# Kernel tuning notes

Hardware: AMD Instinct MI355X
Metric: run time of the kernel (lower is better)

## Reference

```python
import jax, jax.numpy as jnp
import numpy as np

BLOCK_SIZES = [256] * 8            # sum = N_CTX = 2048
B, H, D = 2, 16, 64
N_CTX = sum(BLOCK_SIZES)
SPARSITY_PATTERN = 'block_causal'  # row_starts = 0, row_ends = end of own block


def _build_masks(block_sizes, pattern):
    cs = np.cumsum([0] + list(block_sizes))
    row_ends = np.concatenate([np.full(bs, cs[i + 1], dtype=np.int32)
                               for i, bs in enumerate(block_sizes)])
    if pattern == 'block_diagonal':
        row_starts = np.concatenate([np.full(bs, cs[i], dtype=np.int32)
                                     for i, bs in enumerate(block_sizes)])
    elif pattern == 'block_causal':
        row_starts = np.zeros_like(row_ends)
    else:
        raise ValueError(pattern)
    return jnp.asarray(row_starts), jnp.asarray(row_ends)


def setup_inputs() -> dict:
    key = jax.random.key(0)
    kq, kk, kv = jax.random.split(key, 3)
    q = jax.random.normal(kq, (B, H, N_CTX, D), dtype=jnp.float32)
    k = jax.random.normal(kk, (B, H, N_CTX, D), dtype=jnp.float32)
    v = jax.random.normal(kv, (B, H, N_CTX, D), dtype=jnp.float32)
    row_starts, row_ends = _build_masks(BLOCK_SIZES, SPARSITY_PATTERN)
    sm_scale = jnp.float32(1.0 / np.sqrt(D))
    return {"q": q, "k": k, "v": v, "sm_scale": sm_scale,
            "row_starts": row_starts, "row_ends": row_ends}


def reference(q, k, v, sm_scale, row_starts, row_ends):
    # q,k,v: [B,H,N,D]; per query row i, attend to kv cols in [row_starts[i], row_ends[i])
    n = q.shape[2]
    cols = jnp.arange(n, dtype=jnp.int32)
    allowed = (cols[None, :] >= row_starts[:, None]) & (cols[None, :] < row_ends[:, None])  # [N,N]
    scores = jnp.einsum('bhqd,bhkd->bhqk', q, k) * sm_scale
    neg = jnp.finfo(scores.dtype).min
    scores = jnp.where(allowed[None, None], scores, neg)
    p = jax.nn.softmax(scores, axis=-1)
    return jnp.einsum('bhqk,bhkd->bhqd', p, v)
```

## Files before the change

### kernel.cpp

```cpp
#include <hip/hip_runtime.h>


typedef short bf16x8 __attribute__((ext_vector_type(8)));
typedef float f32x4  __attribute__((ext_vector_type(4)));
typedef unsigned short u16;
typedef u16 u16x8 __attribute__((ext_vector_type(8)));

#define MFMA(A,B,C) __builtin_amdgcn_mfma_f32_16x16x32_bf16((A),(B),(C),0,0,0)

__device__ __forceinline__ u16 f2bf_rne(float f) {
    union { float f; unsigned u; } c; c.f = f;
    unsigned r = c.u + 0x7FFFu + ((c.u >> 16) & 1u);
    return (u16)(r >> 16);
}
__device__ __forceinline__ u16 f2bf_fast(float f) {
    union { float f; unsigned u; } c; c.f = f;
    return (u16)((c.u + 0x8000u) >> 16);
}

__global__ __launch_bounds__(512, 2)
void bsattn_fused(const float* __restrict__ Q, const float* __restrict__ K,
                  const float* __restrict__ V, const float* __restrict__ SC,
                  const int* __restrict__ RS, const int* __restrict__ RE,
                  float* __restrict__ O)
{
    constexpr int N = 2048, D = 64;
    int wg = blockIdx.x;
    int lo = wg & 255, hi = wg >> 8;
    int qs = lo >> 4;
    int qsub = hi ? (15 - qs) : qs;
    int bh   = (lo & 15) + (hi << 4);
    int q0 = qsub << 7;

    int tid = threadIdx.x;
    int grp = tid >> 8;
    int tl  = tid & 255;
    int wid = tl >> 6, lane = tl & 63;
    int n = lane & 15, g = lane >> 4;

    __shared__ __align__(16) u16 lsm[32768];
    __shared__ int sbi[16];

    int row0 = q0 + wid * 32 + n;
    int row1 = row0 + 16;
    int rs_l0 = RS[row0], re_l0 = RE[row0];
    int rs_l1 = RS[row1], re_l1 = RE[row1];
    int w_rs_min = min(rs_l0, rs_l1), w_rs_max = max(rs_l0, rs_l1);
    int w_re_min = min(re_l0, re_l1), w_re_max = max(re_l0, re_l1);
    #pragma unroll
    for (int o = 1; o < 16; o <<= 1) {
        w_rs_min = min(w_rs_min, __shfl_xor(w_rs_min, o));
        w_rs_max = max(w_rs_max, __shfl_xor(w_rs_max, o));
        w_re_min = min(w_re_min, __shfl_xor(w_re_min, o));
        w_re_max = max(w_re_max, __shfl_xor(w_re_max, o));
    }
    int wid8 = tid >> 6;
    if (lane == 0) { sbi[wid8 * 2] = w_rs_min; sbi[wid8 * 2 + 1] = w_re_max; }

    float sscale = SC[0] * 1.44269504088896340736f;

    bf16x8 qA0, qA1, qB0, qB1;
    {
        const float* qp = Q + ((size_t)bh * N + row0) * D + g * 8;
        float4 a0 = *(const float4*)qp,        a1 = *(const float4*)(qp + 4);
        float4 b0 = *(const float4*)(qp + 32), b1 = *(const float4*)(qp + 36);
        qA0[0]=f2bf_rne(a0.x*sscale); qA0[1]=f2bf_rne(a0.y*sscale);
        qA0[2]=f2bf_rne(a0.z*sscale); qA0[3]=f2bf_rne(a0.w*sscale);
        qA0[4]=f2bf_rne(a1.x*sscale); qA0[5]=f2bf_rne(a1.y*sscale);
        qA0[6]=f2bf_rne(a1.z*sscale); qA0[7]=f2bf_rne(a1.w*sscale);
        qA1[0]=f2bf_rne(b0.x*sscale); qA1[1]=f2bf_rne(b0.y*sscale);
        qA1[2]=f2bf_rne(b0.z*sscale); qA1[3]=f2bf_rne(b0.w*sscale);
        qA1[4]=f2bf_rne(b1.x*sscale); qA1[5]=f2bf_rne(b1.y*sscale);
        qA1[6]=f2bf_rne(b1.z*sscale); qA1[7]=f2bf_rne(b1.w*sscale);
    }
    {
        const float* qp = Q + ((size_t)bh * N + row1) * D + g * 8;
        float4 a0 = *(const float4*)qp,        a1 = *(const float4*)(qp + 4);
        float4 b0 = *(const float4*)(qp + 32), b1 = *(const float4*)(qp + 36);
        qB0[0]=f2bf_rne(a0.x*sscale); qB0[1]=f2bf_rne(a0.y*sscale);
        qB0[2]=f2bf_rne(a0.z*sscale); qB0[3]=f2bf_rne(a0.w*sscale);
        qB0[4]=f2bf_rne(a1.x*sscale); qB0[5]=f2bf_rne(a1.y*sscale);
        qB0[6]=f2bf_rne(a1.z*sscale); qB0[7]=f2bf_rne(a1.w*sscale);
        qB1[0]=f2bf_rne(b0.x*sscale); qB1[1]=f2bf_rne(b0.y*sscale);
        qB1[2]=f2bf_rne(b0.z*sscale); qB1[3]=f2bf_rne(b0.w*sscale);
        qB1[4]=f2bf_rne(b1.x*sscale); qB1[5]=f2bf_rne(b1.y*sscale);
        qB1[6]=f2bf_rne(b1.z*sscale); qB1[7]=f2bf_rne(b1.w*sscale);
    }

    __syncthreads();
    int kst  = min(min(min(sbi[0], sbi[2]),  min(sbi[4],  sbi[6])),
                   min(min(sbi[8], sbi[10]), min(sbi[12], sbi[14]))) & ~63;
    int kend = max(max(max(sbi[1], sbi[3]),  max(sbi[5],  sbi[7])),
                   max(max(sbi[9], sbi[11]), max(sbi[13], sbi[15])));
    int t0 = kst >> 6;
    int w  = (kend - kst + 63) >> 6;
    int wl = w >> 1;

    int rA   = ((n >> 2) << 3) + (n & 3);
    int phk  = (n & 3) + 4 * ((n >> 2) & 1);
    int osA0 = rA * 64 + ((g + phk) & 7) * 8;
    int osA1 = rA * 64 + ((g + 4 + phk) & 7) * 8;
    int ov0  = 4096 + n * 64 + ((    g + (n & 7)) & 7) * 8;
    int ov1  = 4096 + n * 64 + ((4 + g + (n & 7)) & 7) * 8;

    int key_l = tl >> 2, c2 = (tl & 3) << 1;
    int rotb  = (key_l & 3) + 4 * ((key_l >> 3) & 1);
    int kiA   = key_l * 64 + (((c2    ) + rotb) & 7) * 8;
    int kiB   = key_l * 64 + (((c2 + 1) + rotb) & 7) * 8;
    int kc    = lane >> 3, kw = lane & 7;
    const float* Kb = K + (size_t)bh * N * D;
    const float* Vb = V + (size_t)bh * N * D;

    int go = grp << 14;

    f32x4 accA[4], accB[4];
    f32x4 acclA = {0.f,0.f,0.f,0.f}, acclB = {0.f,0.f,0.f,0.f};
    #pragma unroll
    for (int c = 0; c < 4; ++c) {
        accA[c] = (f32x4){0.f,0.f,0.f,0.f};
        accB[c] = (f32x4){0.f,0.f,0.f,0.f};
    }
    bf16x8 ones;
    #pragma unroll
    for (int j = 0; j < 8; ++j) ones[j] = (short)0x3F80;

    float4 kf0, kf1, kf2, kf3, vf0, vf1, vf2, vf3;

    auto stage_load = [&](int i) {
        if (i < wl) {
            int tile = t0 + grp * wl + i;
            const float* kp = Kb + (size_t)tile * 4096 + key_l * 64 + c2 * 8;
            kf0 = *(const float4*)kp;       kf1 = *(const float4*)(kp + 4);
            kf2 = *(const float4*)(kp + 8); kf3 = *(const float4*)(kp + 12);
            const float* vp = Vb + (size_t)tile * 4096 + lane * 64 + wid * 16;
            vf0 = *(const float4*)vp;       vf1 = *(const float4*)(vp + 4);
            vf2 = *(const float4*)(vp + 8); vf3 = *(const float4*)(vp + 12);
        }
    };
    auto stage_write = [&](int i) {
        if (i < wl) {
            u16* dst = &lsm[go + ((i & 1) << 13)];
            u16x8 a, b;
            a[0]=f2bf_rne(kf0.x); a[1]=f2bf_rne(kf0.y); a[2]=f2bf_rne(kf0.z); a[3]=f2bf_rne(kf0.w);
            a[4]=f2bf_rne(kf1.x); a[5]=f2bf_rne(kf1.y); a[6]=f2bf_rne(kf1.z); a[7]=f2bf_rne(kf1.w);
            b[0]=f2bf_rne(kf2.x); b[1]=f2bf_rne(kf2.y); b[2]=f2bf_rne(kf2.z); b[3]=f2bf_rne(kf2.w);
            b[4]=f2bf_rne(kf3.x); b[5]=f2bf_rne(kf3.y); b[6]=f2bf_rne(kf3.z); b[7]=f2bf_rne(kf3.w);
            *(u16x8*)&dst[kiA] = a;
            *(u16x8*)&dst[kiB] = b;
            float vy[16] = { vf0.x,vf0.y,vf0.z,vf0.w, vf1.x,vf1.y,vf1.z,vf1.w,
                             vf2.x,vf2.y,vf2.z,vf2.w, vf3.x,vf3.y,vf3.z,vf3.w };
            #pragma unroll
            for (int j = 0; j < 16; ++j) {
                int d = wid * 16 + j;
                dst[4096 + d * 64 + ((kc + (j & 7)) & 7) * 8 + kw] = f2bf_rne(vy[j]);
            }
        }
    };

    auto proc = [&](int kb, const u16* ls) {
        bool bdry = (kb < w_rs_max) || (kb + 64 > w_re_min);
        #pragma unroll
        for (int h = 0; h < 2; ++h) {
            int hb = h * 2048;
            bf16x8 k00 = *(const bf16x8*)&ls[hb + osA0];
            bf16x8 k01 = *(const bf16x8*)&ls[hb + osA1];
            bf16x8 k10 = *(const bf16x8*)&ls[hb + osA0 + 256];
            bf16x8 k11 = *(const bf16x8*)&ls[hb + osA1 + 256];
            f32x4 tA0 = {0.f,0.f,0.f,0.f}, tA1 = tA0, tB0 = tA0, tB1 = tA0;
            __builtin_amdgcn_s_setprio(1);
            tA0 = MFMA(k00, qA0, tA0); tA0 = MFMA(k01, qA1, tA0);
            tA1 = MFMA(k10, qA0, tA1); tA1 = MFMA(k11, qA1, tA1);
            tB0 = MFMA(k00, qB0, tB0); tB0 = MFMA(k01, qB1, tB0);
            tB1 = MFMA(k10, qB0, tB1); tB1 = MFMA(k11, qB1, tB1);
            __builtin_amdgcn_s_setprio(0);
            float sA[8], sB[8];
            #pragma unroll
            for (int r = 0; r < 4; ++r) {
                sA[r] = tA0[r]; sA[4 + r] = tA1[r];
                sB[r] = tB0[r]; sB[4 + r] = tB1[r];
            }
            if (bdry) {
                #pragma unroll
                for (int j = 0; j < 8; ++j) {
                    int key = kb + h * 32 + g * 8 + j;
                    if (key < rs_l0 || key >= re_l0) sA[j] = -1e30f;
                    if (key < rs_l1 || key >= re_l1) sB[j] = -1e30f;
                }
            }
            bf16x8 pA, pB;
            #pragma unroll
            for (int j = 0; j < 8; ++j) { float p = __builtin_amdgcn_exp2f(sA[j]); pA[j] = (short)f2bf_fast(p); }
            #pragma unroll
            for (int j = 0; j < 8; ++j) { float p = __builtin_amdgcn_exp2f(sB[j]); pB[j] = (short)f2bf_fast(p); }
            int ov = h ? ov1 : ov0;
            bf16x8 v0 = *(const bf16x8*)&ls[ov       ];
            bf16x8 v1 = *(const bf16x8*)&ls[ov + 1024];
            bf16x8 v2 = *(const bf16x8*)&ls[ov + 2048];
            bf16x8 v3 = *(const bf16x8*)&ls[ov + 3072];
            __builtin_amdgcn_s_setprio(1);
            accA[0] = MFMA(pA, v0, accA[0]);
            accA[1] = MFMA(pA, v1, accA[1]);
            accA[2] = MFMA(pA, v2, accA[2]);
            accA[3] = MFMA(pA, v3, accA[3]);
            acclA   = MFMA(pA, ones, acclA);
            accB[0] = MFMA(pB, v0, accB[0]);
            accB[1] = MFMA(pB, v1, accB[1]);
            accB[2] = MFMA(pB, v2, accB[2]);
            accB[3] = MFMA(pB, v3, accB[3]);
            acclB   = MFMA(pB, ones, acclB);
            __builtin_amdgcn_s_setprio(0);
        }
    };

    stage_load(0);
    stage_write(0);
    for (int i = 0; i < wl; ++i) {
        __syncthreads();
        stage_load(i + 1);
        proc(kst + ((grp * wl + i) << 6), &lsm[go + ((i & 1) << 13)]);
        stage_write(i + 1);
    }

    __syncthreads();
    float* mf = (float*)lsm;
    if (grp == 1) {
        int slot = tl * 41;
        #pragma unroll
        for (int c = 0; c < 4; ++c)
            #pragma unroll
            for (int r = 0; r < 4; ++r) mf[slot + c * 4 + r] = accA[c][r];
        #pragma unroll
        for (int r = 0; r < 4; ++r) mf[slot + 16 + r] = acclA[r];
        #pragma unroll
        for (int c = 0; c < 4; ++c)
            #pragma unroll
            for (int r = 0; r < 4; ++r) mf[slot + 20 + c * 4 + r] = accB[c][r];
        #pragma unroll
        for (int r = 0; r < 4; ++r) mf[slot + 36 + r] = acclB[r];
    }
    __syncthreads();
    if (grp == 0) {
        int slot = tl * 41;
        #pragma unroll
        for (int c = 0; c < 4; ++c)
            #pragma unroll
            for (int r = 0; r < 4; ++r) accA[c][r] += mf[slot + c * 4 + r];
        #pragma unroll
        for (int r = 0; r < 4; ++r) acclA[r] += mf[slot + 16 + r];
        #pragma unroll
        for (int c = 0; c < 4; ++c)
            #pragma unroll
            for (int r = 0; r < 4; ++r) accB[c][r] += mf[slot + 20 + c * 4 + r];
        #pragma unroll
        for (int r = 0; r < 4; ++r) acclB[r] += mf[slot + 36 + r];

        int rb = g << 2;
        {
            int orow = q0 + wid * 32 + rb;
            float* ob = O + ((size_t)bh * N + orow) * D + n;
            #pragma unroll
            for (int r = 0; r < 4; ++r) {
                float li = 1.0f / acclA[r];
                float* rp = ob + (size_t)r * D;
                rp[0]  = accA[0][r] * li;
                rp[16] = accA[1][r] * li;
                rp[32] = accA[2][r] * li;
                rp[48] = accA[3][r] * li;
            }
        }
        {
            int orow = q0 + wid * 32 + 16 + rb;
            float* ob = O + ((size_t)bh * N + orow) * D + n;
            #pragma unroll
            for (int r = 0; r < 4; ++r) {
                float li = 1.0f / acclB[r];
                float* rp = ob + (size_t)r * D;
                rp[0]  = accB[0][r] * li;
                rp[16] = accB[1][r] * li;
                rp[32] = accB[2][r] * li;
                rp[48] = accB[3][r] * li;
            }
        }
    }
}

extern "C" void kernel_launch(void* const* d_in, const int* in_sizes, int n_in,
                              void* d_out, int out_size, void* d_ws, size_t ws_size,
                              hipStream_t stream) {
    const float* q  = (const float*)d_in[0];
    const float* k  = (const float*)d_in[1];
    const float* v  = (const float*)d_in[2];
    const float* sc = (const float*)d_in[3];
    const int* rs   = (const int*)d_in[4];
    const int* re   = (const int*)d_in[5];
    float* out      = (float*)d_out;

    bsattn_fused<<<dim3(512), dim3(512), 0, stream>>>(q, k, v, sc, rs, re, out);
}
```

Measured before the change: 127.7 us.

## Deepen K/V global prefetch to two tiles with ping-pong register sets

K and V now use two register sets, so each tile is loaded from global memory two iterations before use instead of one. The LDS write for the next tile now happens right after the barrier and before the compute on the current tile, rather than after it. The aim is to hide more global load latency behind the MFMA work. The cost is 32 more VGPRs under a launch bound of 512 threads with 2 blocks per CU, plus runtime selects between the two register sets, which could cause spills or extra instructions.

```diff
diff --git a/kernel.cpp b/kernel.cpp
--- a/kernel.cpp
+++ b/kernel.cpp
@@ -124,31 +124,42 @@
     #pragma unroll
     for (int j = 0; j < 8; ++j) ones[j] = (short)0x3F80;
 
-    float4 kf0, kf1, kf2, kf3, vf0, vf1, vf2, vf3;
-
-    auto stage_load = [&](int i) {
-        if (i < wl) {
-            int tile = t0 + grp * wl + i;
+    float4 kA0, kA1, kA2, kA3, vA0, vA1, vA2, vA3;
+    float4 kB0, kB1, kB2, kB3, vB0, vB1, vB2, vB3;
+
+    auto stage_load = [&](int t) {
+        if (t < wl) {
+            int tile = t0 + grp * wl + t;
             const float* kp = Kb + (size_t)tile * 4096 + key_l * 64 + c2 * 8;
-            kf0 = *(const float4*)kp;       kf1 = *(const float4*)(kp + 4);
-            kf2 = *(const float4*)(kp + 8); kf3 = *(const float4*)(kp + 12);
             const float* vp = Vb + (size_t)tile * 4096 + lane * 64 + wid * 16;
-            vf0 = *(const float4*)vp;       vf1 = *(const float4*)(vp + 4);
-            vf2 = *(const float4*)(vp + 8); vf3 = *(const float4*)(vp + 12);
+            if (t & 1) {
+                kB0 = *(const float4*)kp;       kB1 = *(const float4*)(kp + 4);
+                kB2 = *(const float4*)(kp + 8); kB3 = *(const float4*)(kp + 12);
+                vB0 = *(const float4*)vp;       vB1 = *(const float4*)(vp + 4);
+                vB2 = *(const float4*)(vp + 8); vB3 = *(const float4*)(vp + 12);
+            } else {
+                kA0 = *(const float4*)kp;       kA1 = *(const float4*)(kp + 4);
+                kA2 = *(const float4*)(kp + 8); kA3 = *(const float4*)(kp + 12);
+                vA0 = *(const float4*)vp;       vA1 = *(const float4*)(vp + 4);
+                vA2 = *(const float4*)(vp + 8); vA3 = *(const float4*)(vp + 12);
+            }
         }
     };
-    auto stage_write = [&](int i) {
-        if (i < wl) {
-            u16* dst = &lsm[go + ((i & 1) << 13)];
+    auto stage_write = [&](int t) {
+        if (t < wl) {
+            u16* dst = &lsm[go + ((t & 1) << 13)];
+            float4 k0, k1, k2, k3, v0, v1, v2, v3;
+            if (t & 1) { k0=kB0; k1=kB1; k2=kB2; k3=kB3; v0=vB0; v1=vB1; v2=vB2; v3=vB3; }
+            else       { k0=kA0; k1=kA1; k2=kA2; k3=kA3; v0=vA0; v1=vA1; v2=vA2; v3=vA3; }
             u16x8 a, b;
-            a[0]=f2bf_rne(kf0.x); a[1]=f2bf_rne(kf0.y); a[2]=f2bf_rne(kf0.z); a[3]=f2bf_rne(kf0.w);
-            a[4]=f2bf_rne(kf1.x); a[5]=f2bf_rne(kf1.y); a[6]=f2bf_rne(kf1.z); a[7]=f2bf_rne(kf1.w);
-            b[0]=f2bf_rne(kf2.x); b[1]=f2bf_rne(kf2.y); b[2]=f2bf_rne(kf2.z); b[3]=f2bf_rne(kf2.w);
-            b[4]=f2bf_rne(kf3.x); b[5]=f2bf_rne(kf3.y); b[6]=f2bf_rne(kf3.z); b[7]=f2bf_rne(kf3.w);
+            a[0]=f2bf_rne(k0.x); a[1]=f2bf_rne(k0.y); a[2]=f2bf_rne(k0.z); a[3]=f2bf_rne(k0.w);
+            a[4]=f2bf_rne(k1.x); a[5]=f2bf_rne(k1.y); a[6]=f2bf_rne(k1.z); a[7]=f2bf_rne(k1.w);
+            b[0]=f2bf_rne(k2.x); b[1]=f2bf_rne(k2.y); b[2]=f2bf_rne(k2.z); b[3]=f2bf_rne(k2.w);
+            b[4]=f2bf_rne(k3.x); b[5]=f2bf_rne(k3.y); b[6]=f2bf_rne(k3.z); b[7]=f2bf_rne(k3.w);
             *(u16x8*)&dst[kiA] = a;
             *(u16x8*)&dst[kiB] = b;
-            float vy[16] = { vf0.x,vf0.y,vf0.z,vf0.w, vf1.x,vf1.y,vf1.z,vf1.w,
-                             vf2.x,vf2.y,vf2.z,vf2.w, vf3.x,vf3.y,vf3.z,vf3.w };
+            float vy[16] = { v0.x,v0.y,v0.z,v0.w, v1.x,v1.y,v1.z,v1.w,
+                             v2.x,v2.y,v2.z,v2.w, v3.x,v3.y,v3.z,v3.w };
             #pragma unroll
             for (int j = 0; j < 16; ++j) {
                 int d = wid * 16 + j;
@@ -213,12 +224,13 @@
     };
 
     stage_load(0);
+    stage_load(1);
     stage_write(0);
     for (int i = 0; i < wl; ++i) {
         __syncthreads();
-        stage_load(i + 1);
+        stage_write(i + 1);
+        stage_load(i + 2);
         proc(kst + ((grp * wl + i) << 6), &lsm[go + ((i & 1) << 13)]);
-        stage_write(i + 1);
     }
 
     __syncthreads();
```

After: 231.8 us. 81.5% more time.
